# Kernel optimization log

Hardware: AMD Instinct MI355X
Metric: run time of the kernel (lower is better)

Reference implementation:

```python
import jax, jax.numpy as jnp
import numpy as np

B, S, HID = 1, 2048, 4096
H, KV, D = 32, 8, 128          # query heads, kv heads, head_dim
THETA = 100000.0               # rope base


def setup_inputs() -> dict:
    key = jax.random.key(0)
    k1, k2, k3, k4, k5 = jax.random.split(key, 5)
    hidden_states = jax.random.normal(k1, (B, S, HID), jnp.float32)
    # W_pack: Linear(hidden, H*D + 2*KV*D), torch weight layout [out, in]
    w_pack = jax.random.normal(k2, (H * D + 2 * KV * D, HID), jnp.float32) * 0.02
    w_o = jax.random.normal(k3, (HID, H * D), jnp.float32) * 0.02
    # conv kernels: per-kv-head causal mixing weights of width 2 (softmax-normalized at init)
    conv_k = jax.nn.softmax(jax.random.normal(k4, (KV, 2), jnp.float32), axis=-1)
    conv_v = jax.nn.softmax(jax.random.normal(k5, (KV, 2), jnp.float32), axis=-1)
    return dict(hidden_states=hidden_states, w_pack=w_pack, w_o=w_o,
                conv_k=conv_k, conv_v=conv_v)


def _causal_conv2(u, k):
    """u: [b,s,h,d], k: [h,2]. v[t] = k[h,0]*u[t-1] + k[h,1]*u[t] (zero pad at t=-1).
    Equivalent to custom_convolution with window 2 (unfold+mul+sum)."""
    prev = jnp.pad(u, ((0, 0), (1, 0), (0, 0), (0, 0)))[:, :-1]
    return k[None, None, :, 0:1] * prev + k[None, None, :, 1:2] * u


def _rope(x):
    """Non-interleaved (half-split) rotary over full head_dim. x: [b,s,h,d]."""
    s, d = x.shape[1], x.shape[-1]
    inv = 1.0 / (THETA ** (jnp.arange(0, d, 2, dtype=jnp.float32) / d))
    freqs = jnp.arange(s, dtype=jnp.float32)[:, None] * inv[None, :]  # [s, d/2]
    cos = jnp.cos(freqs)[None, :, None, :]
    sin = jnp.sin(freqs)[None, :, None, :]
    x1, x2 = x[..., : d // 2], x[..., d // 2:]
    return jnp.concatenate([x1 * cos - x2 * sin, x1 * sin + x2 * cos], axis=-1)


def reference(hidden_states, w_pack, w_o, conv_k, conv_v):
    qkv = hidden_states @ w_pack.T                       # [b,s,H*D+2*KV*D]
    q = qkv[..., : H * D].reshape(B, S, H, D)
    k = qkv[..., H * D: H * D + KV * D].reshape(B, S, KV, D)
    v = qkv[..., H * D + KV * D:].reshape(B, S, KV, D)

    # causal depthwise width-2 conv mixing on K and V (prefill path)
    k = _causal_conv2(k, conv_k)
    v = _causal_conv2(v, conv_v)

    # rotary on q, k
    q = _rope(q)
    k = _rope(k)

    # GQA: repeat kv heads to match query heads
    g = H // KV
    k = jnp.repeat(k, g, axis=2)
    v = jnp.repeat(v, g, axis=2)

    scale = 1.0 / np.sqrt(D).astype(np.float32)
    scores = jnp.einsum('bqhd,bkhd->bhqk', q, k) * scale  # [b,H,S,S]
    causal = jnp.tril(jnp.ones((S, S), dtype=bool))
    scores = jnp.where(causal[None, None], scores, jnp.finfo(scores.dtype).min)
    probs = jax.nn.softmax(scores, axis=-1)
    out = jnp.einsum('bhqk,bkhd->bqhd', probs, v).reshape(B, S, H * D)
    return out @ w_o.T
```

## Files before the change

kernel.cpp:

```cpp
#include <hip/hip_runtime.h>
#include <hip/hip_bf16.h>

#define S_LEN 2048
#define HID 4096
#define NH 32
#define NKV 8
#define HD 128

typedef unsigned short u16;
typedef __attribute__((ext_vector_type(4))) float f32x4;
typedef __attribute__((ext_vector_type(8))) short bf16x8;

__device__ __forceinline__ u16 f2bf(float x) {
  union { float f; unsigned u; } c; c.f = x;
  unsigned r = c.u + 0x7FFFu + ((c.u >> 16) & 1u);
  return (u16)(r >> 16);
}

__device__ __forceinline__ float bf2f(u16 x) {
  union { unsigned u; float f; } c; c.u = (unsigned)x << 16;
  return c.f;
}

__device__ __forceinline__ void gload16(const void* g, void* l) {
  __builtin_amdgcn_global_load_lds(
      (const __attribute__((address_space(1))) unsigned int*)g,
      (__attribute__((address_space(3))) unsigned int*)l, 16, 0, 0);
}

__device__ __forceinline__ unsigned cvtpk_bf16(float lo, float hi) {
  unsigned r;
  asm("v_cvt_pk_bf16_f32 %0, %1, %2" : "=v"(r) : "v"(lo), "v"(hi));
  return r;
}

__device__ __forceinline__ float bcastf(float v, int srclane) {
  int r = __builtin_amdgcn_ds_bpermute(srclane << 2, __builtin_bit_cast(int, v));
  return __builtin_bit_cast(float, r);
}

__global__ void cvt4_kernel(const float* __restrict__ s, u16* __restrict__ d, int n4) {
  int i = blockIdx.x * 256 + threadIdx.x;
  if (i >= n4) return;
  float4 v = ((const float4*)s)[i];
  ushort4 o;
  o.x = f2bf(v.x); o.y = f2bf(v.y); o.z = f2bf(v.z); o.w = f2bf(v.w);
  ((ushort4*)d)[i] = o;
}

__global__ void rope_tab_kernel(float2* __restrict__ tab) {
  int i = blockIdx.x * 256 + threadIdx.x;
  int t = i >> 6, d = i & 63;
  float inv = expf(-(float)d * (11.512925464970229f / 64.0f));
  float f = (float)t * inv;
  float2 cs; cs.x = cosf(f); cs.y = sinf(f);
  tab[i] = cs;
}

__global__ void rope_q_kernel(const u16* __restrict__ qkv, const float* __restrict__ tab,
                              u16* __restrict__ Q) {
  int i = blockIdx.x * 256 + threadIdx.x;
  int d4 = (i & 15) * 4, h = (i >> 4) & 31, t = i >> 9;
  const u16* row = qkv + (size_t)t * 6144 + h * 128;
  ushort4 a = *(const ushort4*)(row + d4);
  ushort4 b = *(const ushort4*)(row + d4 + 64);
  const float4* tf = (const float4*)(tab + ((t << 6) + d4) * 2);
  float4 c01 = tf[0], c23 = tf[1];
  const float SC = 0.12752551286084f;
  float x10 = bf2f(a.x), x11 = bf2f(a.y), x12 = bf2f(a.z), x13 = bf2f(a.w);
  float x20 = bf2f(b.x), x21 = bf2f(b.y), x22 = bf2f(b.z), x23 = bf2f(b.w);
  ushort4 o1, o2;
  o1.x = f2bf((x10 * c01.x - x20 * c01.y) * SC);
  o1.y = f2bf((x11 * c01.z - x21 * c01.w) * SC);
  o1.z = f2bf((x12 * c23.x - x22 * c23.y) * SC);
  o1.w = f2bf((x13 * c23.z - x23 * c23.w) * SC);
  o2.x = f2bf((x10 * c01.y + x20 * c01.x) * SC);
  o2.y = f2bf((x11 * c01.w + x21 * c01.z) * SC);
  o2.z = f2bf((x12 * c23.y + x22 * c23.x) * SC);
  o2.w = f2bf((x13 * c23.w + x23 * c23.z) * SC);
  u16* orow = Q + (((size_t)t * NH + h) << 7);
  *(ushort4*)(orow + d4) = o1;
  *(ushort4*)(orow + d4 + 64) = o2;
}

__global__ void convrope_k_kernel(const u16* __restrict__ qkv, const float* __restrict__ ck,
                                  const float* __restrict__ tab, u16* __restrict__ K) {
  int i = blockIdx.x * 256 + threadIdx.x;
  int d4 = (i & 15) * 4, kv = (i >> 4) & 7, t = i >> 7;
  const u16* cur = qkv + (size_t)t * 6144 + 4096 + kv * 128;
  float c0 = ck[kv * 2], c1 = ck[kv * 2 + 1];
  ushort4 a = *(const ushort4*)(cur + d4);
  ushort4 b = *(const ushort4*)(cur + d4 + 64);
  float x1[4] = { c1 * bf2f(a.x), c1 * bf2f(a.y), c1 * bf2f(a.z), c1 * bf2f(a.w) };
  float x2[4] = { c1 * bf2f(b.x), c1 * bf2f(b.y), c1 * bf2f(b.z), c1 * bf2f(b.w) };
  if (t > 0) {
    const u16* prv = cur - 6144;
    ushort4 pa = *(const ushort4*)(prv + d4);
    ushort4 pb = *(const ushort4*)(prv + d4 + 64);
    x1[0] += c0 * bf2f(pa.x); x1[1] += c0 * bf2f(pa.y); x1[2] += c0 * bf2f(pa.z); x1[3] += c0 * bf2f(pa.w);
    x2[0] += c0 * bf2f(pb.x); x2[1] += c0 * bf2f(pb.y); x2[2] += c0 * bf2f(pb.z); x2[3] += c0 * bf2f(pb.w);
  }
  const float4* tf = (const float4*)(tab + ((t << 6) + d4) * 2);
  float4 c01 = tf[0], c23 = tf[1];
  float cs[4] = { c01.x, c01.z, c23.x, c23.z };
  float sn[4] = { c01.y, c01.w, c23.y, c23.w };
  ushort4 o1, o2;
  o1.x = f2bf(x1[0] * cs[0] - x2[0] * sn[0]);
  o1.y = f2bf(x1[1] * cs[1] - x2[1] * sn[1]);
  o1.z = f2bf(x1[2] * cs[2] - x2[2] * sn[2]);
  o1.w = f2bf(x1[3] * cs[3] - x2[3] * sn[3]);
  o2.x = f2bf(x1[0] * sn[0] + x2[0] * cs[0]);
  o2.y = f2bf(x1[1] * sn[1] + x2[1] * cs[1]);
  o2.z = f2bf(x1[2] * sn[2] + x2[2] * cs[2]);
  o2.w = f2bf(x1[3] * sn[3] + x2[3] * cs[3]);
  u16* orow = K + (((size_t)t * NKV + kv) << 7);
  *(ushort4*)(orow + d4) = o1;
  *(ushort4*)(orow + d4 + 64) = o2;
}

__global__ __launch_bounds__(256) void convT_v_kernel(const u16* __restrict__ qkv,
                                                      const float* __restrict__ cv,
                                                      u16* __restrict__ VT) {
  __shared__ u16 ld[65][128];
  int tt = blockIdx.x * 64, kv = blockIdx.y;
  float c0 = cv[kv * 2], c1 = cv[kv * 2 + 1];
  for (int idx = threadIdx.x; idx < 65 * 32; idx += 256) {
    int r = idx >> 5, d4 = (idx & 31) * 4;
    int t = tt - 1 + r;
    ushort4 v = (t >= 0) ? *(const ushort4*)(qkv + (size_t)t * 6144 + 5120 + kv * 128 + d4)
                         : (ushort4){0, 0, 0, 0};
    *(ushort4*)(&ld[r][d4]) = v;
  }
  __syncthreads();
  int d = threadIdx.x >> 1, tc = (threadIdx.x & 1) * 32;
  u16* out = VT + ((size_t)kv * 128 + d) * S_LEN + tt + tc;
#pragma unroll
  for (int j = 0; j < 32; ++j)
    out[j] = f2bf(c0 * bf2f(ld[tc + j][d]) + c1 * bf2f(ld[tc + j + 1][d]));
}

#define BM 128
#define BN 128
#define BK 64

template <bool BF16OUT>
__global__ __launch_bounds__(256, 2) void gemm_nt_kernel(const u16* __restrict__ A,
                                                         const u16* __restrict__ B,
                                                         void* __restrict__ C,
                                                         int M, int N, int K) {
  __shared__ __align__(16) u16 lA[BM * BK];
  __shared__ __align__(16) u16 lB[BN * BK];
  const int tid = threadIdx.x;
  const int wid = tid >> 6, lane = tid & 63;
  const int bm = blockIdx.y * BM, bn = blockIdx.x * BN;
  const int wr = (wid >> 1) * 64, wc = (wid & 1) * 64;
  const int lr = lane & 15, lg = lane >> 4;
  f32x4 acc[4][4] = {};
  const char* Ab = (const char*)A;
  const char* Bb = (const char*)B;
  const int nk = K / BK;
  for (int kt = 0; kt < nk; ++kt) {
    const size_t k0b = (size_t)kt * (BK * 2);
    __syncthreads();
#pragma unroll
    for (int i = 0; i < 4; ++i) {
      int off = (i * 4 + wid) * 1024 + lane * 16;
      int row = off >> 7, inrow = off & 127;
      int sw = inrow ^ ((row & 7) << 4);
      gload16(Ab + (size_t)(bm + row) * (K * 2) + k0b + sw, (char*)lA + (i * 4 + wid) * 1024);
      gload16(Bb + (size_t)(bn + row) * (K * 2) + k0b + sw, (char*)lB + (i * 4 + wid) * 1024);
    }
    __syncthreads();
    bf16x8 af[4][2], bfv[4][2];
#pragma unroll
    for (int m = 0; m < 4; ++m)
#pragma unroll
      for (int ks = 0; ks < 2; ++ks) {
        int row = wr + m * 16 + lr;
        int boff = row * 128 + ((ks * 64 + lg * 16) ^ ((row & 7) << 4));
        af[m][ks] = *(const bf16x8*)((const char*)lA + boff);
      }
#pragma unroll
    for (int n = 0; n < 4; ++n)
#pragma unroll
      for (int ks = 0; ks < 2; ++ks) {
        int row = wc + n * 16 + lr;
        int boff = row * 128 + ((ks * 64 + lg * 16) ^ ((row & 7) << 4));
        bfv[n][ks] = *(const bf16x8*)((const char*)lB + boff);
      }
#pragma unroll
    for (int m = 0; m < 4; ++m)
#pragma unroll
      for (int n = 0; n < 4; ++n)
#pragma unroll
        for (int ks = 0; ks < 2; ++ks)
          acc[m][n] = __builtin_amdgcn_mfma_f32_16x16x32_bf16(af[m][ks], bfv[n][ks], acc[m][n], 0, 0, 0);
  }
#pragma unroll
  for (int m = 0; m < 4; ++m)
#pragma unroll
    for (int n = 0; n < 4; ++n)
#pragma unroll
      for (int r = 0; r < 4; ++r) {
        int row = bm + wr + m * 16 + lg * 4 + r;
        int col = bn + wc + n * 16 + lr;
        if (BF16OUT)
          ((u16*)C)[(size_t)row * N + col] = f2bf(acc[m][n][r]);
        else
          ((float*)C)[(size_t)row * N + col] = acc[m][n][r];
      }
}

__global__ __launch_bounds__(256, 2) void attn_kernel(const u16* __restrict__ Q,
                                                      const u16* __restrict__ K,
                                                      const u16* __restrict__ VT,
                                                      u16* __restrict__ O) {
  __shared__ __align__(16) u16 lK[2][64 * 128];
  __shared__ __align__(16) u16 lV[2][128 * 64];
  __shared__ __align__(16) u16 lP[4][2][16 * 64];
  const int tid = threadIdx.x;
  const int wid = tid >> 6, lane = tid & 63;
  const int lr = lane & 15, lg = lane >> 4;
  const int g = blockIdx.x;
  const int s = g & 255;
  const int h = s >> 3, j = s & 7;
  const int b = (g < 256) ? (15 - j) : j;
  const int kvh = h >> 2;
  const int qtA = 2 * b, qtB = 2 * b + 1;
  const int qrowA = qtA * 64 + wid * 16 + lr;
  const int qrowB = qtB * 64 + wid * 16 + lr;

  bf16x8 qfA[4], qfB[4];
#pragma unroll
  for (int ks = 0; ks < 4; ++ks) {
    qfA[ks] = *(const bf16x8*)(Q + (((size_t)qrowA * NH + h) << 7) + ks * 32 + lg * 8);
    qfB[ks] = *(const bf16x8*)(Q + (((size_t)qrowB * NH + h) << 7) + ks * 32 + lg * 8);
  }

  f32x4 oA[8] = {}, oB[8] = {};
  float mA = -1e30f, sumA = 0.f, mB = -1e30f, sumB = 0.f;

  const char* Kb = (const char*)K;
  const char* Vb = (const char*)VT;
  char* pbA = (char*)lP[wid][0];
  char* pbB = (char*)lP[wid][1];

  auto stage = [&](int buf, int kt) {
    char* dK = (char*)lK[buf];
    char* dV = (char*)lV[buf];
#pragma unroll
    for (int i = 0; i < 4; ++i) {
      int off = (i * 4 + wid) * 1024 + lane * 16;
      int t = off >> 8, inrow = off & 255;
      gload16(Kb + (((size_t)((kt * 64 + t) * NKV + kvh)) << 8) + (inrow ^ ((t & 7) << 4)),
              dK + (i * 4 + wid) * 1024);
      int d = off >> 7, inr2 = off & 127;
      gload16(Vb + ((size_t)(kvh * 128 + d)) * (S_LEN * 2) + kt * 128 + (inr2 ^ ((d & 7) << 4)),
              dV + (i * 4 + wid) * 1024);
    }
  };

  auto smx = [&](f32x4* sv, float& mm, float& ll, f32x4* o, char* pbuf, bool diag, int qrow, int kt) {
    if (diag) {
#pragma unroll
      for (int n = 0; n < 4; ++n)
#pragma unroll
        for (int r = 0; r < 4; ++r) {
          int kg = kt * 64 + n * 16 + lg * 4 + r;
          if (kg > qrow) sv[n][r] = -1e30f;
        }
    }
    float pm = sv[0][0];
#pragma unroll
    for (int n = 0; n < 4; ++n)
#pragma unroll
      for (int r = 0; r < 4; ++r) pm = fmaxf(pm, sv[n][r]);
    pm = fmaxf(pm, __shfl_xor(pm, 16));
    pm = fmaxf(pm, __shfl_xor(pm, 32));
    if (__any(pm > mm + 8.f)) {
      float mn = fmaxf(mm, pm);
      float al = exp2f(mm - mn);
      mm = mn;
      ll *= al;
      float alo[4];
#pragma unroll
      for (int r = 0; r < 4; ++r) alo[r] = bcastf(al, lg * 4 + r);
#pragma unroll
      for (int nt = 0; nt < 8; ++nt)
#pragma unroll
        for (int r = 0; r < 4; ++r) o[nt][r] *= alo[r];
    }
    float rs = 0.f;
#pragma unroll
    for (int n = 0; n < 4; ++n)
#pragma unroll
      for (int r = 0; r < 4; ++r) {
        float p = exp2f(sv[n][r] - mm);
        sv[n][r] = p;
        rs += p;
      }
    rs += __shfl_xor(rs, 16);
    rs += __shfl_xor(rs, 32);
    ll += rs;
#pragma unroll
    for (int n = 0; n < 4; ++n) {
      uint2 w;
      w.x = cvtpk_bf16(sv[n][0], sv[n][1]);
      w.y = cvtpk_bf16(sv[n][2], sv[n][3]);
      *(uint2*)(pbuf + ((lr * 128 + n * 32 + lg * 8) ^ ((lr & 7) << 4))) = w;
    }
  };

  stage(0, 0);
  __syncthreads();
  for (int kt = 0; kt <= qtB; ++kt) {
    int cur = kt & 1;
    if (kt < qtB) stage(cur ^ 1, kt + 1);
    const char* kb = (const char*)lK[cur];
    const char* vb = (const char*)lV[cur];
    const bool doA = (kt <= qtA);

    f32x4 svA[4], svB[4];
#pragma unroll
    for (int n = 0; n < 4; ++n) {
      f32x4 aA = {}, aB = {};
#pragma unroll
      for (int ks = 0; ks < 4; ++ks) {
        int trow = n * 16 + lr;
        int boff = trow * 256 + ((ks * 64 + lg * 16) ^ ((trow & 7) << 4));
        bf16x8 kf = *(const bf16x8*)(kb + boff);
        aB = __builtin_amdgcn_mfma_f32_16x16x32_bf16(kf, qfB[ks], aB, 0, 0, 0);
        aA = __builtin_amdgcn_mfma_f32_16x16x32_bf16(kf, qfA[ks], aA, 0, 0, 0);
      }
      svA[n] = aA; svB[n] = aB;
    }

    if (doA) smx(svA, mA, sumA, oA, pbA, kt == qtA, qrowA, kt);
    smx(svB, mB, sumB, oB, pbB, kt == qtB, qrowB, kt);

#pragma unroll
    for (int ks = 0; ks < 2; ++ks) {
      int poff = (lr * 128 + 64 * ks + 16 * lg) ^ ((lr & 7) << 4);
      bf16x8 pfB = *(const bf16x8*)(pbB + poff);
      bf16x8 pfA = *(const bf16x8*)(pbA + poff);
#pragma unroll
      for (int nt = 0; nt < 8; ++nt) {
        int drow = nt * 16 + lr;
        int vboff = drow * 128 + ((ks * 64 + lg * 16) ^ ((drow & 7) << 4));
        bf16x8 vf = *(const bf16x8*)(vb + vboff);
        oB[nt] = __builtin_amdgcn_mfma_f32_16x16x32_bf16(pfB, vf, oB[nt], 0, 0, 0);
        if (doA) oA[nt] = __builtin_amdgcn_mfma_f32_16x16x32_bf16(pfA, vf, oA[nt], 0, 0, 0);
      }
    }
    __syncthreads();
  }

  float riA = 1.0f / sumA, riB = 1.0f / sumB;
  float rA[4], rB[4];
#pragma unroll
  for (int r = 0; r < 4; ++r) {
    rA[r] = bcastf(riA, lg * 4 + r);
    rB[r] = bcastf(riB, lg * 4 + r);
  }
#pragma unroll
  for (int nt = 0; nt < 8; ++nt)
#pragma unroll
    for (int r = 0; r < 4; ++r) {
      int rowA = qtA * 64 + wid * 16 + lg * 4 + r;
      int rowB = qtB * 64 + wid * 16 + lg * 4 + r;
      int col = nt * 16 + lr;
      O[(size_t)rowA * 4096 + h * 128 + col] = f2bf(oA[nt][r] * rA[r]);
      O[(size_t)rowB * 4096 + h * 128 + col] = f2bf(oB[nt][r] * rB[r]);
    }
}

extern "C" void kernel_launch(void* const* d_in, const int* in_sizes, int n_in,
                              void* d_out, int out_size, void* d_ws, size_t ws_size,
                              hipStream_t stream) {
  const float* hidden = (const float*)d_in[0];
  const float* wpack  = (const float*)d_in[1];
  const float* wo     = (const float*)d_in[2];
  const float* convk  = (const float*)d_in[3];
  const float* convv  = (const float*)d_in[4];
  float* out = (float*)d_out;

  char* w = (char*)d_ws;
  u16*  hiddenB = (u16*)w;
  u16*  wpackB  = (u16*)(w + 16777216);
  u16*  qkvB    = (u16*)(w + 67108864);
  u16*  qrope   = (u16*)(w + 92274688);
  u16*  krope   = (u16*)(w + 109051904);
  u16*  vT      = (u16*)(w + 113246208);
  float* tab    = (float*)(w + 117440512);

  cvt4_kernel<<<8192, 256, 0, stream>>>(hidden, hiddenB, 2097152);
  cvt4_kernel<<<24576, 256, 0, stream>>>(wpack, wpackB, 6291456);
  rope_tab_kernel<<<512, 256, 0, stream>>>((float2*)tab);
  gemm_nt_kernel<true><<<dim3(48, 16), 256, 0, stream>>>(hiddenB, wpackB, qkvB, 2048, 6144, 4096);
  cvt4_kernel<<<16384, 256, 0, stream>>>(wo, wpackB, 4194304);
  rope_q_kernel<<<4096, 256, 0, stream>>>(qkvB, tab, qrope);
  convrope_k_kernel<<<1024, 256, 0, stream>>>(qkvB, convk, tab, krope);
  convT_v_kernel<<<dim3(32, 8), 256, 0, stream>>>(qkvB, convv, vT);
  attn_kernel<<<512, 256, 0, stream>>>(qrope, krope, vT, hiddenB);
  gemm_nt_kernel<false><<<dim3(32, 16), 256, 0, stream>>>(hiddenB, wpackB, out, 2048, 4096, 4096);
}
```

Baseline: 485.7 us.

## Double-buffer LDS tiles in GEMM to overlap global loads with MFMA

Restructures the NT GEMM main loop to use two LDS buffers, prefetching the tile two steps ahead via direct-to-LDS loads while MFMAs consume fragments already in registers. Uses explicit vmcnt/lgkmcnt waits and raw s_barrier instead of __syncthreads, and raises wave priority around the MFMA block. This aims to hide global memory latency, at the cost of doubling LDS use per block (64KB), which may limit the two-blocks-per-CU occupancy.

```diff
diff --git a/kernel.cpp b/kernel.cpp
--- a/kernel.cpp
+++ b/kernel.cpp
@@ -148,8 +148,8 @@
                                                          const u16* __restrict__ B,
                                                          void* __restrict__ C,
                                                          int M, int N, int K) {
-  __shared__ __align__(16) u16 lA[BM * BK];
-  __shared__ __align__(16) u16 lB[BN * BK];
+  __shared__ __align__(16) u16 lA[2][BM * BK];
+  __shared__ __align__(16) u16 lB[2][BN * BK];
   const int tid = threadIdx.x;
   const int wid = tid >> 6, lane = tid & 63;
   const int bm = blockIdx.y * BM, bn = blockIdx.x * BN;
@@ -159,43 +159,68 @@
   const char* Ab = (const char*)A;
   const char* Bb = (const char*)B;
   const int nk = K / BK;
-  for (int kt = 0; kt < nk; ++kt) {
+
+  auto stage = [&](int buf, int kt) {
     const size_t k0b = (size_t)kt * (BK * 2);
-    __syncthreads();
 #pragma unroll
     for (int i = 0; i < 4; ++i) {
       int off = (i * 4 + wid) * 1024 + lane * 16;
       int row = off >> 7, inrow = off & 127;
       int sw = inrow ^ ((row & 7) << 4);
-      gload16(Ab + (size_t)(bm + row) * (K * 2) + k0b + sw, (char*)lA + (i * 4 + wid) * 1024);
-      gload16(Bb + (size_t)(bn + row) * (K * 2) + k0b + sw, (char*)lB + (i * 4 + wid) * 1024);
-    }
-    __syncthreads();
-    bf16x8 af[4][2], bfv[4][2];
+      gload16(Ab + (size_t)(bm + row) * (K * 2) + k0b + sw, (char*)lA[buf] + (i * 4 + wid) * 1024);
+      gload16(Bb + (size_t)(bn + row) * (K * 2) + k0b + sw, (char*)lB[buf] + (i * 4 + wid) * 1024);
+    }
+  };
+
+  bf16x8 af[8], bfv[8];
+  auto rdfrags = [&](int buf) {
 #pragma unroll
     for (int m = 0; m < 4; ++m)
 #pragma unroll
       for (int ks = 0; ks < 2; ++ks) {
-        int row = wr + m * 16 + lr;
-        int boff = row * 128 + ((ks * 64 + lg * 16) ^ ((row & 7) << 4));
-        af[m][ks] = *(const bf16x8*)((const char*)lA + boff);
-      }
-#pragma unroll
-    for (int n = 0; n < 4; ++n)
-#pragma unroll
-      for (int ks = 0; ks < 2; ++ks) {
-        int row = wc + n * 16 + lr;
-        int boff = row * 128 + ((ks * 64 + lg * 16) ^ ((row & 7) << 4));
-        bfv[n][ks] = *(const bf16x8*)((const char*)lB + boff);
-      }
+        int rowa = wr + m * 16 + lr;
+        int boffa = rowa * 128 + ((ks * 64 + lg * 16) ^ ((rowa & 7) << 4));
+        af[m * 2 + ks] = *(const bf16x8*)((const char*)lA[buf] + boffa);
+        int rowb = wc + m * 16 + lr;
+        int boffb = rowb * 128 + ((ks * 64 + lg * 16) ^ ((rowb & 7) << 4));
+        bfv[m * 2 + ks] = *(const bf16x8*)((const char*)lB[buf] + boffb);
+      }
+  };
+
+  stage(0, 0);
+  stage(1, 1);
+  asm volatile("s_waitcnt vmcnt(8)" ::: "memory");
+  __builtin_amdgcn_s_barrier();
+  rdfrags(0);
+  asm volatile("s_waitcnt lgkmcnt(0)" ::: "memory");
+  __builtin_amdgcn_s_barrier();
+
+  int cur = 0;
+  for (int kt = 0; kt < nk; ++kt) {
+    if (kt + 2 < nk) stage(cur, kt + 2);
+    __builtin_amdgcn_s_setprio(1);
 #pragma unroll
     for (int m = 0; m < 4; ++m)
 #pragma unroll
       for (int n = 0; n < 4; ++n)
 #pragma unroll
         for (int ks = 0; ks < 2; ++ks)
-          acc[m][n] = __builtin_amdgcn_mfma_f32_16x16x32_bf16(af[m][ks], bfv[n][ks], acc[m][n], 0, 0, 0);
-  }
+          acc[m][n] = __builtin_amdgcn_mfma_f32_16x16x32_bf16(af[m * 2 + ks], bfv[n * 2 + ks], acc[m][n], 0, 0, 0);
+    __builtin_amdgcn_s_setprio(0);
+    if (kt + 1 < nk) {
+      if (kt + 2 < nk) {
+        asm volatile("s_waitcnt vmcnt(8)" ::: "memory");
+      } else {
+        asm volatile("s_waitcnt vmcnt(0)" ::: "memory");
+      }
+      __builtin_amdgcn_s_barrier();
+      rdfrags(cur ^ 1);
+      asm volatile("s_waitcnt lgkmcnt(0)" ::: "memory");
+      __builtin_amdgcn_s_barrier();
+    }
+    cur ^= 1;
+  }
+
 #pragma unroll
   for (int m = 0; m < 4; ++m)
 #pragma unroll
```

Result: no change. 488.2 us (+0.5%).
